# Performance work log

Measured on AMD Instinct MI355X. Metric: run time of the kernel, lower is better.

The kernel has to match this reference:

```python
import jax, jax.numpy as jnp
import numpy as np

N, IN_DIM, OUT_DIM = 8192, 512, 256
ALPHA = 0.2
NEG_INF = -9e15


def setup_inputs() -> dict:
    key = jax.random.key(0)
    k1, k2, k3, k4 = jax.random.split(key, 4)
    node_features = jax.random.normal(k1, (N, IN_DIM), dtype=jnp.float32)
    adj_matrix = jax.random.randint(k2, (N, N), 0, 2, dtype=jnp.int32)
    # xavier-uniform linear weight [out,in] -> store as [in,out]
    lim_w = float(np.sqrt(6.0 / (IN_DIM + OUT_DIM)))
    W = jax.random.uniform(k3, (IN_DIM, OUT_DIM), dtype=jnp.float32, minval=-lim_w, maxval=lim_w)
    b = jnp.zeros((OUT_DIM,), dtype=jnp.float32)
    # attention Linear(2*out_dim, 1): weight a [2*out_dim], bias scalar
    lim_a = float(np.sqrt(6.0 / (2 * OUT_DIM + 1)))
    a = jax.random.uniform(k4, (2 * OUT_DIM,), dtype=jnp.float32, minval=-lim_a, maxval=lim_a)
    a_bias = jnp.zeros((), dtype=jnp.float32)
    return {"adj_matrix": adj_matrix, "node_features": node_features, "W": W, "b": b, "a": a, "a_bias": a_bias}


def reference(adj_matrix, node_features, W, b, a, a_bias):
    # h = Linear(node_features); dropout is identity in eval mode
    h = node_features @ W + b                     # [N, D]
    # attention(cat(h_i, h_j)) == h_i @ a_l + h_j @ a_r + a_bias
    a_l, a_r = a[:OUT_DIM], a[OUT_DIM:]
    e_l = h @ a_l                                 # [N]
    e_r = h @ a_r                                 # [N]
    e = jax.nn.leaky_relu(e_l[:, None] + e_r[None, :] + a_bias, ALPHA)  # [N, N]
    scores = jnp.where(adj_matrix > 0, e, NEG_INF)
    attention = jax.nn.softmax(scores, axis=1)    # [N, N]
    h_prime = attention @ h                       # [N, D]
    return h_prime
```

## Files before the change

### kernel.cpp

```cpp
#include <hip/hip_runtime.h>

#define N 8192
#define DIN 512
#define DOUT 256
#define ALPHA 0.2f
#define NEG_INF -9.0e15f

typedef __attribute__((ext_vector_type(8))) short bf16x8;
typedef __attribute__((ext_vector_type(4))) float f32x4;
typedef __attribute__((ext_vector_type(4))) int   i32x4;

__device__ __forceinline__ unsigned f2bf_u(float f) {
    unsigned u = __builtin_bit_cast(unsigned, f);
    return (u + 0x7fffu + ((u >> 16) & 1u)) >> 16;
}
__device__ __forceinline__ unsigned pack2bf(float lo, float hi) {
    return f2bf_u(lo) | (f2bf_u(hi) << 16);
}
union U4BF8 { uint4 u; bf16x8 v; };

__device__ __forceinline__ void async_copy16(const ushort* g, ushort* l) {
    __builtin_amdgcn_global_load_lds(
        (const __attribute__((address_space(1))) unsigned*)g,
        (__attribute__((address_space(3))) unsigned*)l, 16, 0, 0);
}

__global__ __launch_bounds__(256) void wb_kernel(const float* __restrict__ W,
                                                 ushort* __restrict__ WB) {
    const int g = blockIdx.x * 256 + threadIdx.x;
    const int c = g & 255, k8 = g >> 8;
    const float* wp = W + (size_t)(k8 * 8) * DOUT + c;
    U4BF8 o;
    o.u.x = pack2bf(wp[0 * DOUT], wp[1 * DOUT]);
    o.u.y = pack2bf(wp[2 * DOUT], wp[3 * DOUT]);
    o.u.z = pack2bf(wp[4 * DOUT], wp[5 * DOUT]);
    o.u.w = pack2bf(wp[6 * DOUT], wp[7 * DOUT]);
    *(uint4*)(WB + (size_t)g * 8) = o.u;
}

__global__ __launch_bounds__(256) void h_kernel(
        const float* __restrict__ X, const ushort* __restrict__ WB,
        const float* __restrict__ bvec, const float* __restrict__ a,
        ushort* __restrict__ hB, float* __restrict__ el, float* __restrict__ er)
{
    __shared__ float red[4][64][65];
    __shared__ float elr[2][4][16];
    const int t = threadIdx.x;
    const int w = t >> 6, l = t & 63, q = l >> 4, n = l & 15;
    const int i0 = blockIdx.x * 16;
    f32x4 acc[16];
    #pragma unroll
    for (int ct = 0; ct < 16; ++ct) acc[ct] = (f32x4){0.f, 0.f, 0.f, 0.f};
    const float* xp = X + (size_t)(i0 + n) * DIN + q * 8;

    #pragma unroll
    for (int ks = 0; ks < 4; ++ks) {
        const int k0 = w * 128 + ks * 32;
        const float4 x0 = *(const float4*)(xp + k0);
        const float4 x1 = *(const float4*)(xp + k0 + 4);
        U4BF8 pa;
        pa.u.x = pack2bf(x0.x, x0.y); pa.u.y = pack2bf(x0.z, x0.w);
        pa.u.z = pack2bf(x1.x, x1.y); pa.u.w = pack2bf(x1.z, x1.w);
        const ushort* wbp = WB + ((k0 >> 3) + q) * 2048 + n * 8;
        bf16x8 bfr[16];
        #pragma unroll
        for (int ct = 0; ct < 16; ++ct) bfr[ct] = *(const bf16x8*)(wbp + ct * 128);
        #pragma unroll
        for (int ct = 0; ct < 16; ++ct)
            acc[ct] = __builtin_amdgcn_mfma_f32_16x16x32_bf16(pa.v, bfr[ct], acc[ct], 0, 0, 0);
    }
    #pragma unroll
    for (int ct = 0; ct < 16; ++ct)
        #pragma unroll
        for (int r = 0; r < 4; ++r) red[w][l][ct * 4 + r] = acc[ct][r];
    __syncthreads();

    float pl[4] = {0.f, 0.f, 0.f, 0.f}, pr[4] = {0.f, 0.f, 0.f, 0.f};
    const int hbase = (blockIdx.x * 2 + (q >> 1)) * 2048 + n * 8 + (q & 1) * 4;
    #pragma unroll
    for (int c2 = 0; c2 < 4; ++c2) {
        const int ct = w * 4 + c2;
        const float bb = bvec[ct * 16 + n];
        const float al = a[ct * 16 + n];
        const float ar = a[DOUT + ct * 16 + n];
        float v[4];
        #pragma unroll
        for (int r = 0; r < 4; ++r) {
            v[r] = red[0][l][ct * 4 + r] + red[1][l][ct * 4 + r]
                 + red[2][l][ct * 4 + r] + red[3][l][ct * 4 + r] + bb;
            pl[r] += v[r] * al;
            pr[r] += v[r] * ar;
        }
        ushort4 hp;
        hp.x = (ushort)f2bf_u(v[0]); hp.y = (ushort)f2bf_u(v[1]);
        hp.z = (ushort)f2bf_u(v[2]); hp.w = (ushort)f2bf_u(v[3]);
        *(ushort4*)&hB[hbase + ct * 128] = hp;
    }
    #pragma unroll
    for (int r = 0; r < 4; ++r) {
        #pragma unroll
        for (int off = 1; off < 16; off <<= 1) {
            pl[r] += __shfl_xor(pl[r], off);
            pr[r] += __shfl_xor(pr[r], off);
        }
    }
    if (n == 0) {
        #pragma unroll
        for (int r = 0; r < 4; ++r) {
            elr[0][w][q * 4 + r] = pl[r];
            elr[1][w][q * 4 + r] = pr[r];
        }
    }
    __syncthreads();
    if (t < 16) {
        el[i0 + t] = elr[0][0][t] + elr[0][1][t] + elr[0][2][t] + elr[0][3][t];
        er[i0 + t] = elr[1][0][t] + elr[1][1][t] + elr[1][2][t] + elr[1][3][t];
    }
}

__global__ __launch_bounds__(512, 1) void attn_kernel(
        const int* __restrict__ adj, const float* __restrict__ el,
        const float* __restrict__ er, const float* __restrict__ ab,
        const ushort* __restrict__ hB, float* __restrict__ out)
{
    __shared__ ushort stage[2][32768];
    const int t = threadIdx.x;
    const int w = t >> 6, l = t & 63, q = l >> 4, n = l & 15;
    const int rg = w >> 2, jq = w & 3;
    const int i0 = blockIdx.x * 32;
    const int row = i0 + rg * 16 + n;
    const float elm = el[row] + ab[0];
    const int jb = jq * 32 + q * 8;
    const int* alp = adj + (size_t)row * N + jb;
    const float* elp = er + jb;

    f32x4 acc[16];
    #pragma unroll
    for (int ct = 0; ct < 16; ++ct) acc[ct] = (f32x4){0.f, 0.f, 0.f, 0.f};
    float lsum = 0.f;

    i32x4 ac0 = __builtin_nontemporal_load((const i32x4*)alp);
    i32x4 ac1 = __builtin_nontemporal_load((const i32x4*)(alp + 4));
    float4 ec0 = *(const float4*)elp;
    float4 ec1 = *(const float4*)(elp + 4);
    {
        const ushort* g = hB + w * 512 + l * 8;
        ushort* lb = &stage[0][w * 512];
        #pragma unroll
        for (int i = 0; i < 8; ++i) async_copy16(g + i * 4096, lb + i * 4096);
    }

    for (int s = 0; s < 64; ++s) {
        __syncthreads();
        const i32x4 aa0 = ac0, aa1 = ac1;
        const float4 ee0 = ec0, ee1 = ec1;
        if (s < 63) {
            const int J0n = (s + 1) * 128;
            ac0 = __builtin_nontemporal_load((const i32x4*)(alp + J0n));
            ac1 = __builtin_nontemporal_load((const i32x4*)(alp + J0n + 4));
            ec0 = *(const float4*)(elp + J0n);
            ec1 = *(const float4*)(elp + J0n + 4);
            const ushort* g = hB + (size_t)(s + 1) * 32768 + w * 512 + l * 8;
            ushort* lb = &stage[(s + 1) & 1][w * 512];
            #pragma unroll
            for (int i = 0; i < 8; ++i) async_copy16(g + i * 4096, lb + i * 4096);
        }
        float v, p0, p1, p2, p3, p4, p5, p6, p7;
        v = elm + ee0.x; v = fmaxf(v, ALPHA * v); p0 = __expf(aa0.x > 0 ? v : NEG_INF);
        v = elm + ee0.y; v = fmaxf(v, ALPHA * v); p1 = __expf(aa0.y > 0 ? v : NEG_INF);
        v = elm + ee0.z; v = fmaxf(v, ALPHA * v); p2 = __expf(aa0.z > 0 ? v : NEG_INF);
        v = elm + ee0.w; v = fmaxf(v, ALPHA * v); p3 = __expf(aa0.w > 0 ? v : NEG_INF);
        v = elm + ee1.x; v = fmaxf(v, ALPHA * v); p4 = __expf(aa1.x > 0 ? v : NEG_INF);
        v = elm + ee1.y; v = fmaxf(v, ALPHA * v); p5 = __expf(aa1.y > 0 ? v : NEG_INF);
        v = elm + ee1.z; v = fmaxf(v, ALPHA * v); p6 = __expf(aa1.z > 0 ? v : NEG_INF);
        v = elm + ee1.w; v = fmaxf(v, ALPHA * v); p7 = __expf(aa1.w > 0 ? v : NEG_INF);
        lsum += p0 + p1 + p2 + p3 + p4 + p5 + p6 + p7;
        U4BF8 pa;
        pa.u.x = pack2bf(p0, p1); pa.u.y = pack2bf(p2, p3);
        pa.u.z = pack2bf(p4, p5); pa.u.w = pack2bf(p6, p7);
        const ushort* sb = &stage[s & 1][(jq * 4 + q) * 2048 + n * 8];
        #pragma unroll
        for (int ct = 0; ct < 16; ++ct) {
            const bf16x8 bf = *(const bf16x8*)(sb + ct * 128);
            acc[ct] = __builtin_amdgcn_mfma_f32_16x16x32_bf16(pa.v, bf, acc[ct], 0, 0, 0);
        }
    }

    lsum += __shfl_xor(lsum, 16);
    lsum += __shfl_xor(lsum, 32);

    float* accbuf = (float*)&stage[0][0];
    float* LpB    = (float*)&stage[1][0];
    float* linvB  = LpB + 128;
    __syncthreads();
    if (l < 16) LpB[(rg * 4 + jq) * 16 + n] = lsum;
    if (jq == 0) {
        #pragma unroll
        for (int ct = 0; ct < 16; ++ct)
            #pragma unroll
            for (int r = 0; r < 4; ++r)
                accbuf[(rg * 16 + q * 4 + r) * 272 + ct * 16 + n] = acc[ct][r];
    }
    __syncthreads();
    if (jq == 1) {
        #pragma unroll
        for (int ct = 0; ct < 16; ++ct)
            #pragma unroll
            for (int r = 0; r < 4; ++r)
                accbuf[(rg * 16 + q * 4 + r) * 272 + ct * 16 + n] += acc[ct][r];
    }
    __syncthreads();
    if (jq == 2) {
        #pragma unroll
        for (int ct = 0; ct < 16; ++ct)
            #pragma unroll
            for (int r = 0; r < 4; ++r)
                accbuf[(rg * 16 + q * 4 + r) * 272 + ct * 16 + n] += acc[ct][r];
    }
    __syncthreads();
    if (jq == 3) {
        #pragma unroll
        for (int ct = 0; ct < 16; ++ct)
            #pragma unroll
            for (int r = 0; r < 4; ++r)
                accbuf[(rg * 16 + q * 4 + r) * 272 + ct * 16 + n] += acc[ct][r];
    }
    __syncthreads();
    if (t < 32) {
        const int rr = t >> 4, m = t & 15;
        linvB[t] = 1.0f / (LpB[(rr * 4 + 0) * 16 + m] + LpB[(rr * 4 + 1) * 16 + m]
                         + LpB[(rr * 4 + 2) * 16 + m] + LpB[(rr * 4 + 3) * 16 + m]);
    }
    __syncthreads();
    const int orow = t >> 4, c0 = (t & 15) * 16;
    const float li = linvB[orow];
    #pragma unroll
    for (int ch = 0; ch < 4; ++ch) {
        float4 vv = *(const float4*)&accbuf[orow * 272 + c0 + ch * 4];
        vv.x *= li; vv.y *= li; vv.z *= li; vv.w *= li;
        *(float4*)&out[(size_t)(i0 + orow) * 256 + c0 + ch * 4] = vv;
    }
}

extern "C" void kernel_launch(void* const* d_in, const int* in_sizes, int n_in,
                              void* d_out, int out_size, void* d_ws, size_t ws_size,
                              hipStream_t stream) {
    const int*   adj = (const int*)  d_in[0];
    const float* X   = (const float*)d_in[1];
    const float* W   = (const float*)d_in[2];
    const float* b   = (const float*)d_in[3];
    const float* a   = (const float*)d_in[4];
    const float* ab  = (const float*)d_in[5];
    float* out = (float*)d_out;

    ushort* hB = (ushort*)d_ws;
    ushort* WB = hB + (size_t)N * DOUT;
    float*  el = (float*)(WB + (size_t)DIN * DOUT);
    float*  er = el + N;

    wb_kernel<<<dim3(64), dim3(256), 0, stream>>>(W, WB);
    h_kernel<<<dim3(N / 16), dim3(256), 0, stream>>>(X, WB, b, a, hB, el, er);
    attn_kernel<<<dim3(N / 32), dim3(512), 0, stream>>>(adj, el, er, ab, hB, out);
}
```

Before: 458.2 us.

## Split attention over key dimension across blocks with separate combine kernel

Restructures the attention kernel so each block handles 128 rows and one quarter of the columns, with each wave owning 16 rows. The previous design had 4 waves share each row group and split the K range inside the block. Each hB tile staged in LDS is now reused by 128 rows instead of 32, which cuts global/L2 traffic for h by a factor of four. The er slice is also cached in shared memory. The in-block cross-wave reduction is replaced by writes of partial outputs and row sums to workspace, and a new combine kernel sums and normalizes them. The trade-off is an extra launch plus roughly 32MB of partial-output write and read traffic.

Result: faster. 418.8 us (-8.6%).

```diff
diff --git a/kernel.cpp b/kernel.cpp
--- a/kernel.cpp
+++ b/kernel.cpp
@@ -121,125 +121,117 @@
 __global__ __launch_bounds__(512, 1) void attn_kernel(
         const int* __restrict__ adj, const float* __restrict__ el,
         const float* __restrict__ er, const float* __restrict__ ab,
-        const ushort* __restrict__ hB, float* __restrict__ out)
+        const ushort* __restrict__ hB, float* __restrict__ pout,
+        float* __restrict__ plsum)
 {
     __shared__ ushort stage[2][32768];
+    __shared__ float ers[2048];
     const int t = threadIdx.x;
     const int w = t >> 6, l = t & 63, q = l >> 4, n = l & 15;
-    const int rg = w >> 2, jq = w & 3;
-    const int i0 = blockIdx.x * 32;
-    const int row = i0 + rg * 16 + n;
+    const int rb = blockIdx.x >> 2, jq = blockIdx.x & 3;
+    const int j0 = jq * 2048;
+    const int row = rb * 128 + w * 16 + n;
     const float elm = el[row] + ab[0];
-    const int jb = jq * 32 + q * 8;
-    const int* alp = adj + (size_t)row * N + jb;
-    const float* elp = er + jb;
+    const int* alp = adj + (size_t)row * N + j0 + q * 8;
 
     f32x4 acc[16];
     #pragma unroll
     for (int ct = 0; ct < 16; ++ct) acc[ct] = (f32x4){0.f, 0.f, 0.f, 0.f};
     float lsum = 0.f;
 
-    i32x4 ac0 = __builtin_nontemporal_load((const i32x4*)alp);
-    i32x4 ac1 = __builtin_nontemporal_load((const i32x4*)(alp + 4));
-    float4 ec0 = *(const float4*)elp;
-    float4 ec1 = *(const float4*)(elp + 4);
+    *(float4*)&ers[t * 4] = *(const float4*)&er[j0 + t * 4];
+    i32x4 a[8];
+    #pragma unroll
+    for (int kg = 0; kg < 4; ++kg) {
+        a[2 * kg]     = __builtin_nontemporal_load((const i32x4*)(alp + kg * 32));
+        a[2 * kg + 1] = __builtin_nontemporal_load((const i32x4*)(alp + kg * 32 + 4));
+    }
     {
-        const ushort* g = hB + w * 512 + l * 8;
-        ushort* lb = &stage[0][w * 512];
+        const ushort* g = hB + (size_t)j0 * 256 + t * 8;
+        ushort* lb = &stage[0][t * 8];
         #pragma unroll
         for (int i = 0; i < 8; ++i) async_copy16(g + i * 4096, lb + i * 4096);
     }
 
-    for (int s = 0; s < 64; ++s) {
+    for (int s = 0; s < 16; ++s) {
         __syncthreads();
-        const i32x4 aa0 = ac0, aa1 = ac1;
-        const float4 ee0 = ec0, ee1 = ec1;
-        if (s < 63) {
-            const int J0n = (s + 1) * 128;
-            ac0 = __builtin_nontemporal_load((const i32x4*)(alp + J0n));
-            ac1 = __builtin_nontemporal_load((const i32x4*)(alp + J0n + 4));
-            ec0 = *(const float4*)(elp + J0n);
-            ec1 = *(const float4*)(elp + J0n + 4);
-            const ushort* g = hB + (size_t)(s + 1) * 32768 + w * 512 + l * 8;
-            ushort* lb = &stage[(s + 1) & 1][w * 512];
+        if (s < 15) {
+            const ushort* g = hB + (size_t)(j0 + (s + 1) * 128) * 256 + t * 8;
+            ushort* lb = &stage[(s + 1) & 1][t * 8];
             #pragma unroll
             for (int i = 0; i < 8; ++i) async_copy16(g + i * 4096, lb + i * 4096);
         }
-        float v, p0, p1, p2, p3, p4, p5, p6, p7;
-        v = elm + ee0.x; v = fmaxf(v, ALPHA * v); p0 = __expf(aa0.x > 0 ? v : NEG_INF);
-        v = elm + ee0.y; v = fmaxf(v, ALPHA * v); p1 = __expf(aa0.y > 0 ? v : NEG_INF);
-        v = elm + ee0.z; v = fmaxf(v, ALPHA * v); p2 = __expf(aa0.z > 0 ? v : NEG_INF);
-        v = elm + ee0.w; v = fmaxf(v, ALPHA * v); p3 = __expf(aa0.w > 0 ? v : NEG_INF);
-        v = elm + ee1.x; v = fmaxf(v, ALPHA * v); p4 = __expf(aa1.x > 0 ? v : NEG_INF);
-        v = elm + ee1.y; v = fmaxf(v, ALPHA * v); p5 = __expf(aa1.y > 0 ? v : NEG_INF);
-        v = elm + ee1.z; v = fmaxf(v, ALPHA * v); p6 = __expf(aa1.z > 0 ? v : NEG_INF);
-        v = elm + ee1.w; v = fmaxf(v, ALPHA * v); p7 = __expf(aa1.w > 0 ? v : NEG_INF);
-        lsum += p0 + p1 + p2 + p3 + p4 + p5 + p6 + p7;
-        U4BF8 pa;
-        pa.u.x = pack2bf(p0, p1); pa.u.y = pack2bf(p2, p3);
-        pa.u.z = pack2bf(p4, p5); pa.u.w = pack2bf(p6, p7);
-        const ushort* sb = &stage[s & 1][(jq * 4 + q) * 2048 + n * 8];
-        #pragma unroll
-        for (int ct = 0; ct < 16; ++ct) {
-            const bf16x8 bf = *(const bf16x8*)(sb + ct * 128);
-            acc[ct] = __builtin_amdgcn_mfma_f32_16x16x32_bf16(pa.v, bf, acc[ct], 0, 0, 0);
+        U4BF8 pa[4];
+        #pragma unroll
+        for (int kg = 0; kg < 4; ++kg) {
+            const float4 e0 = *(const float4*)&ers[s * 128 + kg * 32 + q * 8];
+            const float4 e1 = *(const float4*)&ers[s * 128 + kg * 32 + q * 8 + 4];
+            const i32x4 a0 = a[2 * kg], a1 = a[2 * kg + 1];
+            float v, p0, p1, p2, p3, p4, p5, p6, p7;
+            v = elm + e0.x; v = fmaxf(v, ALPHA * v); p0 = __expf(a0.x > 0 ? v : NEG_INF);
+            v = elm + e0.y; v = fmaxf(v, ALPHA * v); p1 = __expf(a0.y > 0 ? v : NEG_INF);
+            v = elm + e0.z; v = fmaxf(v, ALPHA * v); p2 = __expf(a0.z > 0 ? v : NEG_INF);
+            v = elm + e0.w; v = fmaxf(v, ALPHA * v); p3 = __expf(a0.w > 0 ? v : NEG_INF);
+            v = elm + e1.x; v = fmaxf(v, ALPHA * v); p4 = __expf(a1.x > 0 ? v : NEG_INF);
+            v = elm + e1.y; v = fmaxf(v, ALPHA * v); p5 = __expf(a1.y > 0 ? v : NEG_INF);
+            v = elm + e1.z; v = fmaxf(v, ALPHA * v); p6 = __expf(a1.z > 0 ? v : NEG_INF);
+            v = elm + e1.w; v = fmaxf(v, ALPHA * v); p7 = __expf(a1.w > 0 ? v : NEG_INF);
+            lsum += p0 + p1 + p2 + p3 + p4 + p5 + p6 + p7;
+            pa[kg].u.x = pack2bf(p0, p1); pa[kg].u.y = pack2bf(p2, p3);
+            pa[kg].u.z = pack2bf(p4, p5); pa[kg].u.w = pack2bf(p6, p7);
+        }
+        if (s < 15) {
+            const int* ap = alp + (s + 1) * 128;
+            #pragma unroll
+            for (int kg = 0; kg < 4; ++kg) {
+                a[2 * kg]     = __builtin_nontemporal_load((const i32x4*)(ap + kg * 32));
+                a[2 * kg + 1] = __builtin_nontemporal_load((const i32x4*)(ap + kg * 32 + 4));
+            }
+        }
+        #pragma unroll
+        for (int kg = 0; kg < 4; ++kg) {
+            const ushort* sb = &stage[s & 1][(kg * 4 + q) * 2048 + n * 8];
+            #pragma unroll
+            for (int ct = 0; ct < 16; ++ct) {
+                const bf16x8 bf = *(const bf16x8*)(sb + ct * 128);
+                acc[ct] = __builtin_amdgcn_mfma_f32_16x16x32_bf16(pa[kg].v, bf, acc[ct], 0, 0, 0);
+            }
         }
     }
 
     lsum += __shfl_xor(lsum, 16);
     lsum += __shfl_xor(lsum, 32);
-
-    float* accbuf = (float*)&stage[0][0];
-    float* LpB    = (float*)&stage[1][0];
-    float* linvB  = LpB + 128;
-    __syncthreads();
-    if (l < 16) LpB[(rg * 4 + jq) * 16 + n] = lsum;
-    if (jq == 0) {
-        #pragma unroll
-        for (int ct = 0; ct < 16; ++ct)
-            #pragma unroll
-            for (int r = 0; r < 4; ++r)
-                accbuf[(rg * 16 + q * 4 + r) * 272 + ct * 16 + n] = acc[ct][r];
-    }
-    __syncthreads();
-    if (jq == 1) {
-        #pragma unroll
-        for (int ct = 0; ct < 16; ++ct)
-            #pragma unroll
-            for (int r = 0; r < 4; ++r)
-                accbuf[(rg * 16 + q * 4 + r) * 272 + ct * 16 + n] += acc[ct][r];
-    }
-    __syncthreads();
-    if (jq == 2) {
-        #pragma unroll
-        for (int ct = 0; ct < 16; ++ct)
-            #pragma unroll
-            for (int r = 0; r < 4; ++r)
-                accbuf[(rg * 16 + q * 4 + r) * 272 + ct * 16 + n] += acc[ct][r];
-    }
-    __syncthreads();
-    if (jq == 3) {
-        #pragma unroll
-        for (int ct = 0; ct < 16; ++ct)
-            #pragma unroll
-            for (int r = 0; r < 4; ++r)
-                accbuf[(rg * 16 + q * 4 + r) * 272 + ct * 16 + n] += acc[ct][r];
-    }
-    __syncthreads();
-    if (t < 32) {
-        const int rr = t >> 4, m = t & 15;
-        linvB[t] = 1.0f / (LpB[(rr * 4 + 0) * 16 + m] + LpB[(rr * 4 + 1) * 16 + m]
-                         + LpB[(rr * 4 + 2) * 16 + m] + LpB[(rr * 4 + 3) * 16 + m]);
-    }
-    __syncthreads();
-    const int orow = t >> 4, c0 = (t & 15) * 16;
-    const float li = linvB[orow];
-    #pragma unroll
-    for (int ch = 0; ch < 4; ++ch) {
-        float4 vv = *(const float4*)&accbuf[orow * 272 + c0 + ch * 4];
-        vv.x *= li; vv.y *= li; vv.z *= li; vv.w *= li;
-        *(float4*)&out[(size_t)(i0 + orow) * 256 + c0 + ch * 4] = vv;
-    }
+    if (l < 16) plsum[(size_t)jq * N + row] = lsum;
+
+    float* pb = pout + ((size_t)jq * N + rb * 128 + w * 16 + q * 4) * 256 + n;
+    #pragma unroll
+    for (int ct = 0; ct < 16; ++ct)
+        #pragma unroll
+        for (int r = 0; r < 4; ++r)
+            __builtin_nontemporal_store(acc[ct][r], pb + (size_t)r * 256 + ct * 16);
+}
+
+__global__ __launch_bounds__(256) void combine_kernel(
+        const float* __restrict__ pout, const float* __restrict__ plsum,
+        float* __restrict__ out)
+{
+    const int t = threadIdx.x;
+    const int row = blockIdx.x * 4 + (t >> 6);
+    const int c = (t & 63) * 4;
+    const size_t idx = (size_t)row * 256 + c;
+    const size_t qs = (size_t)N * 256;
+    float4 v0 = *(const float4*)&pout[idx];
+    float4 v1 = *(const float4*)&pout[idx + qs];
+    float4 v2 = *(const float4*)&pout[idx + 2 * qs];
+    float4 v3 = *(const float4*)&pout[idx + 3 * qs];
+    const float li = 1.0f / (plsum[row] + plsum[N + row]
+                           + plsum[2 * N + row] + plsum[3 * N + row]);
+    float4 o;
+    o.x = (v0.x + v1.x + v2.x + v3.x) * li;
+    o.y = (v0.y + v1.y + v2.y + v3.y) * li;
+    o.z = (v0.z + v1.z + v2.z + v3.z) * li;
+    o.w = (v0.w + v1.w + v2.w + v3.w) * li;
+    *(float4*)&out[idx] = o;
 }
 
 extern "C" void kernel_launch(void* const* d_in, const int* in_sizes, int n_in,
@@ -253,12 +245,15 @@
     const float* ab  = (const float*)d_in[5];
     float* out = (float*)d_out;
 
-    ushort* hB = (ushort*)d_ws;
-    ushort* WB = hB + (size_t)N * DOUT;
-    float*  el = (float*)(WB + (size_t)DIN * DOUT);
-    float*  er = el + N;
+    ushort* hB    = (ushort*)d_ws;
+    ushort* WB    = hB + (size_t)N * DOUT;
+    float*  el    = (float*)(WB + (size_t)DIN * DOUT);
+    float*  er    = el + N;
+    float*  plsum = er + N;
+    float*  pout  = plsum + 4 * N;
 
     wb_kernel<<<dim3(64), dim3(256), 0, stream>>>(W, WB);
     h_kernel<<<dim3(N / 16), dim3(256), 0, stream>>>(X, WB, b, a, hB, el, er);
-    attn_kernel<<<dim3(N / 32), dim3(512), 0, stream>>>(adj, el, er, ab, hB, out);
-}
+    attn_kernel<<<dim3(256), dim3(512), 0, stream>>>(adj, el, er, ab, hB, pout, plsum);
+    combine_kernel<<<dim3(N / 4), dim3(256), 0, stream>>>(pout, plsum, out);
+}
```
